# Kernel tuning notes

Measured on AMD Instinct MI355X. Metric: run time of the kernel, lower is better.

The kernel has to match this reference:

```python
import jax, jax.numpy as jnp
import numpy as np

N_NODES = 100000
N_EDGES = 1600000
IN_DIM = 256
HIDDEN = 128
N_CLASSES = 10


def setup_inputs() -> dict:
    key = jax.random.key(0)
    k1, k2, k3, k4 = jax.random.split(key, 4)
    x = jax.random.normal(k1, (N_NODES, IN_DIM), dtype=jnp.float32)
    edge_index = jax.random.randint(k2, (2, N_EDGES), 0, N_NODES, dtype=jnp.int64)
    # Glorot-ish init for weights
    W1 = jax.random.normal(k3, (IN_DIM, HIDDEN), dtype=jnp.float32) * (1.0 / np.sqrt(IN_DIM))
    b1 = jnp.zeros((HIDDEN,), dtype=jnp.float32)
    W2 = jax.random.normal(k4, (HIDDEN, N_CLASSES), dtype=jnp.float32) * (1.0 / np.sqrt(HIDDEN))
    b2 = jnp.zeros((N_CLASSES,), dtype=jnp.float32)
    return {"x": x, "edge_index": edge_index, "W1": W1, "b1": b1, "W2": W2, "b2": b2}


def _gcn_norm(edge_index, num_nodes):
    # PyG gcn_norm with add_self_loops=False, edge_weight=1:
    # deg over destination (col), norm = d^-1/2[src] * d^-1/2[dst]
    row, col = edge_index[0], edge_index[1]
    deg = jax.ops.segment_sum(jnp.ones((edge_index.shape[1],), jnp.float32), col,
                              num_segments=num_nodes)
    dinv = jnp.where(deg > 0, jax.lax.rsqrt(jnp.maximum(deg, 1.0)), 0.0)
    return dinv[row] * dinv[col]


def _gcn_conv(x, W, b, row, col, norm, num_nodes):
    h = x @ W                              # [N, out] dense transform
    msg = h[row] * norm[:, None]           # gather + scale, [E, out]
    out = jax.ops.segment_sum(msg, col, num_segments=num_nodes)  # scatter-add
    return out + b


def reference(x, edge_index, W1, b1, W2, b2):
    row, col = edge_index[0], edge_index[1]
    norm = _gcn_norm(edge_index, N_NODES)
    h = _gcn_conv(x, W1, b1, row, col, norm, N_NODES)
    h = jax.nn.relu(h)  # dropout is identity in eval mode
    out = _gcn_conv(h, W2, b2, row, col, norm, N_NODES)
    return out
```

## Files before the change

### kernel.cpp

```cpp
#include <hip/hip_runtime.h>
#include <hip/hip_fp16.h>

typedef _Float16 f16x8 __attribute__((ext_vector_type(8)));
typedef _Float16 f16x2 __attribute__((ext_vector_type(2)));
typedef float f32x4 __attribute__((ext_vector_type(4)));

#define NBUK_MAX 512
#define CHUNK 4096
#define BUKCAP 6144
#define WPAD 264
#define W1T_BLOCKS 64
#define BSTR 16


__global__ __launch_bounds__(512) void k_fat1(const float* __restrict__ W1,
                                              __half* __restrict__ W1T,
                                              const int* __restrict__ row,
                                              const int* __restrict__ col,
                                              int* __restrict__ bcur,
                                              unsigned* __restrict__ pairs,
                                              int E, int nbuk) {
    __shared__ int hist[NBUK_MAX];
    __shared__ int scanA[NBUK_MAX];
    __shared__ int scanB[NBUK_MAX];
    __shared__ int cur[NBUK_MAX];
    __shared__ int gpos[NBUK_MAX];
    __shared__ unsigned staged[CHUNK];
    int tid = threadIdx.x;

    if (blockIdx.x < W1T_BLOCKS) {
        int idx = blockIdx.x * 512 + tid;
        int c = idx >> 8, k = idx & 255;
        W1T[(size_t)c * 256 + k] = __float2half(W1[(size_t)k * 128 + c]);
        return;
    }

    int bid = blockIdx.x - W1T_BLOCKS;
    int e0 = bid * CHUNK;
    int nv = E - e0; if (nv > CHUNK) nv = CHUNK;

    hist[tid] = 0;
    __syncthreads();
    if (nv == CHUNK) {
        const int4* c4 = (const int4*)(col + e0);
#pragma unroll
        for (int it = 0; it < 2; ++it) {
            int4 v = c4[tid + it * 512];
            atomicAdd(&hist[v.x >> 8], 1);
            atomicAdd(&hist[v.y >> 8], 1);
            atomicAdd(&hist[v.z >> 8], 1);
            atomicAdd(&hist[v.w >> 8], 1);
        }
    } else {
        for (int i = tid; i < nv; i += 512) atomicAdd(&hist[col[e0 + i] >> 8], 1);
    }
    __syncthreads();
    int hv = hist[tid];
    scanA[tid] = hv;
    __syncthreads();
    int* pa = scanA;
    int* pb = scanB;
    for (int off = 1; off < 512; off <<= 1) {
        pb[tid] = pa[tid] + ((tid >= off) ? pa[tid - off] : 0);
        __syncthreads();
        int* sw = pa; pa = pb; pb = sw;
    }
    int ex = pa[tid] - hv;
    __syncthreads();
    pb[tid] = ex;
    cur[tid] = ex;
    if (tid < nbuk && hv > 0) gpos[tid] = atomicAdd(&bcur[tid * BSTR], hv);
    __syncthreads();
    int* excl = pb;
    if (nv == CHUNK) {
        const int4* c4 = (const int4*)(col + e0);
        const int4* r4 = (const int4*)(row + e0);
#pragma unroll
        for (int it = 0; it < 2; ++it) {
            int4 c = c4[tid + it * 512];
            int4 r = r4[tid + it * 512];
            int rk;
            rk = atomicAdd(&cur[c.x >> 8], 1); staged[rk] = ((unsigned)(c.x & 255) << 17) | (unsigned)r.x;
            rk = atomicAdd(&cur[c.y >> 8], 1); staged[rk] = ((unsigned)(c.y & 255) << 17) | (unsigned)r.y;
            rk = atomicAdd(&cur[c.z >> 8], 1); staged[rk] = ((unsigned)(c.z & 255) << 17) | (unsigned)r.z;
            rk = atomicAdd(&cur[c.w >> 8], 1); staged[rk] = ((unsigned)(c.w & 255) << 17) | (unsigned)r.w;
        }
    } else {
        for (int i = tid; i < nv; i += 512) {
            int c = col[e0 + i], r = row[e0 + i];
            int rk = atomicAdd(&cur[c >> 8], 1);
            staged[rk] = ((unsigned)(c & 255) << 17) | (unsigned)r;
        }
    }
    __syncthreads();
    int grp = tid >> 4, l16 = tid & 15;
    for (int b = grp; b < nbuk; b += 32) {
        int cnt = hist[b];
        if (cnt == 0) continue;
        int bs = excl[b];
        int gp = gpos[b];
        unsigned* dst = pairs + (size_t)b * BUKCAP;
        for (int l = l16; l < cnt; l += 16) {
            int d = gp + l;
            if (d < BUKCAP) dst[d] = staged[bs + l];
        }
    }
}


__global__ __launch_bounds__(256) void k_csr2a(const unsigned* __restrict__ pairs,
                                               const int* __restrict__ bcur,
                                               int* __restrict__ colptr,
                                               float* __restrict__ dinv,
                                               int N, int E) {
    __shared__ int fc[256];
    __shared__ int cp[256];
    __shared__ int tp[256];
    __shared__ int sA[NBUK_MAX];
    __shared__ int sB[NBUK_MAX];
    int b = blockIdx.x;
    int c0 = b << 8;
    int tid = threadIdx.x;
    fc[tid] = 0;
#pragma unroll
    for (int q = 0; q < 2; ++q) {
        int i = tid + q * 256;
        sA[i] = bcur[i * BSTR];
    }
    __syncthreads();
    int* pa = sA;
    int* pb = sB;
    for (int off = 1; off < 512; off <<= 1) {
#pragma unroll
        for (int q = 0; q < 2; ++q) {
            int i = tid + q * 256;
            pb[i] = pa[i] + ((i >= off) ? pa[i - off] : 0);
        }
        __syncthreads();
        int* sw = pa; pa = pb; pb = sw;
    }
    int cntb = bcur[b * BSTR];
    int p0 = pa[b] - cntb;
    int cnt = cntb > BUKCAP ? BUKCAP : cntb;
    __syncthreads();

    const unsigned* pbk = pairs + (size_t)b * BUKCAP;
    for (int i = tid; i < cnt; i += 256) {
        atomicAdd(&fc[pbk[i] >> 17], 1);
    }
    __syncthreads();
    int deg = fc[tid];
    cp[tid] = deg;
    __syncthreads();
    pa = cp; pb = tp;
    for (int off = 1; off < 256; off <<= 1) {
        pb[tid] = pa[tid] + ((tid >= off) ? pa[tid - off] : 0);
        __syncthreads();
        int* sw = pa; pa = pb; pb = sw;
    }
    int excl = pa[tid] - deg;
    if (c0 + tid < N) {
        colptr[c0 + tid] = p0 + excl;
        dinv[c0 + tid] = (deg > 0) ? rsqrtf((float)deg) : 0.0f;
    }
    if (b == 0 && tid == 0) colptr[N] = E;
}


#define SMEM_BYTES (128 * WPAD * 2)

__global__ __launch_bounds__(512, 4) void k_fat2(const unsigned* __restrict__ pairs,
                                                 const int* __restrict__ bcur,
                                                 const int* __restrict__ colptr,
                                                 int* __restrict__ srcs,
                                                 const float* __restrict__ x,
                                                 const __half* __restrict__ W1T,
                                                 const float* __restrict__ dinv,
                                                 __half* __restrict__ h,
                                                 int N, int nbuk) {
    __shared__ __align__(16) char smem[SMEM_BYTES];
    int tid = threadIdx.x;

    if (blockIdx.x < nbuk) {
        int* tp  = (int*)smem;
        int* fc  = tp + 256;
        int* loc = fc + 256;
        int b = blockIdx.x;
        int c0 = b << 8;
        int cnt = bcur[b * BSTR];
        if (cnt > BUKCAP) cnt = BUKCAP;
        int p0 = colptr[c0];
        if (tid < 256) {
            fc[tid] = 0;
            tp[tid] = (c0 + tid < N) ? (colptr[c0 + tid] - p0) : 0;
        }
        __syncthreads();
        const unsigned* pbk = pairs + (size_t)b * BUKCAP;
        for (int i = tid; i < cnt; i += 512) {
            unsigned v = pbk[i];
            int cl = (int)(v >> 17);
            int r = (int)(v & 0x1FFFFu);
            int off = tp[cl] + atomicAdd(&fc[cl], 1);
            if (off < BUKCAP) loc[off] = r;
            else srcs[p0 + off] = r;
        }
        __syncthreads();
        for (int i = tid; i < cnt; i += 512) srcs[p0 + i] = loc[i];
        return;
    }

    __half (*wt)[WPAD] = (__half(*)[WPAD])smem;
    int gb = blockIdx.x - nbuk;
    int w = tid >> 6, l = tid & 63;
    int r16 = l & 15, kg = l >> 4;
    int r0 = gb * 128;
    int rowi = r0 + w * 16 + r16;
    int rl = (rowi < N) ? rowi : 0;
    const float4* xp = (const float4*)x + (size_t)rl * 64 + kg * 2;

    float4 xr[8];
#pragma unroll
    for (int p = 0; p < 4; ++p) {
        xr[2 * p]     = xp[p * 8];
        xr[2 * p + 1] = xp[p * 8 + 1];
    }

#pragma unroll
    for (int it = 0; it < 8; ++it) {
        int idx = tid + it * 512;
        int c = idx >> 5, q = idx & 31;
        *(float4*)&wt[c][q * 8] = ((const float4*)W1T)[(size_t)c * 32 + q];
    }
    __syncthreads();

    f32x4 acc[8];
#pragma unroll
    for (int n = 0; n < 8; ++n) acc[n] = (f32x4){0.f, 0.f, 0.f, 0.f};

#pragma unroll
    for (int ks = 0; ks < 8; ++ks) {
        float4 c0 = xr[2 * (ks & 3)];
        float4 c1 = xr[2 * (ks & 3) + 1];
        if (ks < 4) {
            xr[2 * (ks & 3)]     = xp[(ks + 4) * 8];
            xr[2 * (ks & 3) + 1] = xp[(ks + 4) * 8 + 1];
        }
        f16x8 a;
        a[0] = (_Float16)c0.x; a[1] = (_Float16)c0.y;
        a[2] = (_Float16)c0.z; a[3] = (_Float16)c0.w;
        a[4] = (_Float16)c1.x; a[5] = (_Float16)c1.y;
        a[6] = (_Float16)c1.z; a[7] = (_Float16)c1.w;
        int kk = ks * 32;
#pragma unroll
        for (int n = 0; n < 8; ++n) {
            f16x8 b = *(const f16x8*)&wt[n * 16 + r16][kk + kg * 8];
            acc[n] = __builtin_amdgcn_mfma_f32_16x16x32_f16(a, b, acc[n], 0, 0, 0);
        }
    }

    float dn[4];
#pragma unroll
    for (int rr = 0; rr < 4; ++rr) {
        int r = r0 + w * 16 + kg * 4 + rr;
        dn[rr] = (r < N) ? dinv[r] : 0.f;
    }
#pragma unroll
    for (int n = 0; n < 8; ++n)
#pragma unroll
        for (int rr = 0; rr < 4; ++rr) {
            int r = r0 + w * 16 + kg * 4 + rr;
            if (r < N)
                h[(size_t)r * 128 + n * 16 + r16] = __float2half(dn[rr] * acc[n][rr]);
        }
}


#define LOAD8(sv, k, vv) { \
    int s0_ = __shfl(sv, (k) + 0), s1_ = __shfl(sv, (k) + 1); \
    int s2_ = __shfl(sv, (k) + 2), s3_ = __shfl(sv, (k) + 3); \
    int s4_ = __shfl(sv, (k) + 4), s5_ = __shfl(sv, (k) + 5); \
    int s6_ = __shfl(sv, (k) + 6), s7_ = __shfl(sv, (k) + 7); \
    vv[0] = hp[(size_t)s0_ * 64 + lane]; vv[1] = hp[(size_t)s1_ * 64 + lane]; \
    vv[2] = hp[(size_t)s2_ * 64 + lane]; vv[3] = hp[(size_t)s3_ * 64 + lane]; \
    vv[4] = hp[(size_t)s4_ * 64 + lane]; vv[5] = hp[(size_t)s5_ * 64 + lane]; \
    vv[6] = hp[(size_t)s6_ * 64 + lane]; vv[7] = hp[(size_t)s7_ * 64 + lane]; }

#define ACC8(vv, A0, A1) { \
    float2 f0_ = __half22float2(vv[0]), f1_ = __half22float2(vv[1]); \
    float2 f2_ = __half22float2(vv[2]), f3_ = __half22float2(vv[3]); \
    float2 f4_ = __half22float2(vv[4]), f5_ = __half22float2(vv[5]); \
    float2 f6_ = __half22float2(vv[6]), f7_ = __half22float2(vv[7]); \
    A0 += ((f0_.x + f1_.x) + (f2_.x + f3_.x)) + ((f4_.x + f5_.x) + (f6_.x + f7_.x)); \
    A1 += ((f0_.y + f1_.y) + (f2_.y + f3_.y)) + ((f4_.y + f5_.y) + (f6_.y + f7_.y)); }

__global__ __launch_bounds__(256) void k_agg1(const __half* __restrict__ h,
                                              const float* __restrict__ dinv,
                                              const int* __restrict__ colptr,
                                              const int* __restrict__ srcs,
                                              const float* __restrict__ b1,
                                              const float* __restrict__ W2,
                                              __half* __restrict__ t, int N) {
    __shared__ __half hs[64][136];
    __shared__ __half w2t[10][136];
    int tid = threadIdx.x;
    int wave = tid >> 6;
    int lane = tid & 63;

    for (int i = tid; i < 1280; i += 256) {
        int c = i >> 7, k = i & 127;
        w2t[c][k] = __float2half(W2[(size_t)k * 10 + c]);
    }

    const __half2* hp = (const __half2*)h;
    int nb0 = blockIdx.x * 64;
    float bb0 = b1[2 * lane], bb1 = b1[2 * lane + 1];

#pragma unroll 1
    for (int i = 0; i < 16; ++i) {
        int n = nb0 + wave * 16 + i;
        if (n >= N) break;
        int jb = colptr[n], je = colptr[n + 1];
        int len = je - jb;
        float a0 = 0.f, a1 = 0.f;
        for (int j0 = 0; j0 < len; j0 += 64) {
            int cnt = len - j0;
            if (cnt > 64) cnt = 64;
            int sv = (lane < cnt) ? srcs[jb + j0 + lane] : 0;
            int k = 0;
            for (; k + 8 <= cnt; k += 8) {
                __half2 va[8];
                LOAD8(sv, k, va);
                ACC8(va, a0, a1);
            }
            for (; k < cnt; ++k) {
                int s = __shfl(sv, k);
                float2 f = __half22float2(hp[(size_t)s * 64 + lane]);
                a0 += f.x; a1 += f.y;
            }
        }
        float dn = dinv[n];
        float v0 = dn * a0 + bb0;
        float v1 = dn * a1 + bb1;
        v0 = v0 > 0.f ? v0 : 0.f;
        v1 = v1 > 0.f ? v1 : 0.f;
        ((__half2*)&hs[wave * 16 + i][0])[lane] = __floats2half2_rn(v0, v1);
    }
    __syncthreads();

#pragma unroll
    for (int it = 0; it < 4; ++it) {
        int idx = tid + it * 256;
        int r = idx >> 4, c = idx & 15;
        int n = nb0 + r;
        if (n < N) {
            float s = 0.f;
            if (c < 10) {
                const float4* hr4 = (const float4*)&hs[r][0];
                const float4* wr4 = (const float4*)&w2t[c][0];
#pragma unroll
                for (int j = 0; j < 16; ++j) {
                    union { float4 v; f16x2 h2[4]; } uh, uw;
                    uh.v = hr4[j];
                    uw.v = wr4[j];
                    s = __builtin_amdgcn_fdot2(uh.h2[0], uw.h2[0], s, false);
                    s = __builtin_amdgcn_fdot2(uh.h2[1], uw.h2[1], s, false);
                    s = __builtin_amdgcn_fdot2(uh.h2[2], uw.h2[2], s, false);
                    s = __builtin_amdgcn_fdot2(uh.h2[3], uw.h2[3], s, false);
                }
                s *= dinv[n];
            }
            t[(size_t)n * 16 + c] = __float2half(s);
        }
    }
}


__global__ __launch_bounds__(256) void k_agg2(const __half* __restrict__ t,
                                              const float* __restrict__ dinv,
                                              const int* __restrict__ colptr,
                                              const int* __restrict__ srcs,
                                              const float* __restrict__ b2,
                                              float* __restrict__ out, int N) {
    int g = threadIdx.x >> 4;
    int lane16 = threadIdx.x & 15;
    int wg = g & 3;
    int n = blockIdx.x * 16 + g;
    if (n >= N) return;
    int jb = colptr[n], je = colptr[n + 1];
    float a = 0.f;
    for (int j0 = jb; j0 < je; j0 += 16) {
        int cnt = je - j0;
        if (cnt > 16) cnt = 16;
        int sv = (lane16 < cnt) ? srcs[j0 + lane16] : 0;
        int k = 0;
        for (; k + 8 <= cnt; k += 8) {
            int s0 = __shfl(sv, wg * 16 + k + 0);
            int s1 = __shfl(sv, wg * 16 + k + 1);
            int s2 = __shfl(sv, wg * 16 + k + 2);
            int s3 = __shfl(sv, wg * 16 + k + 3);
            int s4 = __shfl(sv, wg * 16 + k + 4);
            int s5 = __shfl(sv, wg * 16 + k + 5);
            int s6 = __shfl(sv, wg * 16 + k + 6);
            int s7 = __shfl(sv, wg * 16 + k + 7);
            float x0 = __half2float(t[(size_t)s0 * 16 + lane16]);
            float x1 = __half2float(t[(size_t)s1 * 16 + lane16]);
            float x2 = __half2float(t[(size_t)s2 * 16 + lane16]);
            float x3 = __half2float(t[(size_t)s3 * 16 + lane16]);
            float x4 = __half2float(t[(size_t)s4 * 16 + lane16]);
            float x5 = __half2float(t[(size_t)s5 * 16 + lane16]);
            float x6 = __half2float(t[(size_t)s6 * 16 + lane16]);
            float x7 = __half2float(t[(size_t)s7 * 16 + lane16]);
            a += ((x0 + x1) + (x2 + x3)) + ((x4 + x5) + (x6 + x7));
        }
        for (; k < cnt; ++k) {
            int s = __shfl(sv, wg * 16 + k);
            a += __half2float(t[(size_t)s * 16 + lane16]);
        }
    }
    if (lane16 < 10) out[(size_t)n * 10 + lane16] = dinv[n] * a + b2[lane16];
}


static inline size_t alignup(size_t x) { return (x + 255) & ~(size_t)255; }

extern "C" void kernel_launch(void* const* d_in, const int* in_sizes, int n_in,
                              void* d_out, int out_size, void* d_ws, size_t ws_size,
                              hipStream_t stream) {
    const float* x  = (const float*)d_in[0];
    const int*   ei = (const int*)d_in[1];
    const float* W1 = (const float*)d_in[2];
    const float* b1 = (const float*)d_in[3];
    const float* W2 = (const float*)d_in[4];
    const float* b2 = (const float*)d_in[5];

    int E = in_sizes[1] / 2;
    int N = in_sizes[0] / 256;
    const int* row = ei;
    const int* col = ei + E;
    int nbuk = (N + 255) >> 8;
    int nbE = (E + CHUNK - 1) / CHUNK;
    int nbG1 = (N + 127) / 128;

    char* ws = (char*)d_ws;
    size_t off = 0;
    int*      colptr = (int*)(ws + off);      off += alignup((size_t)(N + 1) * 4);
    float*    dinv   = (float*)(ws + off);    off += alignup((size_t)N * 4);
    int*      bcur   = (int*)(ws + off);      off += alignup((size_t)NBUK_MAX * BSTR * 4);
    int*      srcs   = (int*)(ws + off);      off += alignup((size_t)E * 4);
    unsigned* pairs  = (unsigned*)(ws + off); off += alignup((size_t)NBUK_MAX * BUKCAP * 4);
    __half*   W1T    = (__half*)(ws + off);   off += alignup((size_t)128 * 256 * 2);
    __half*   h      = (__half*)(ws + off);   off += alignup((size_t)N * 128 * 2);
    __half*   t      = (__half*)(ws + off);   off += alignup((size_t)N * 16 * 2);

    hipMemsetAsync(bcur, 0, (size_t)NBUK_MAX * BSTR * 4, stream);

    k_fat1<<<W1T_BLOCKS + nbE, 512, 0, stream>>>(W1, W1T, row, col, bcur, pairs, E, nbuk);
    k_csr2a<<<nbuk, 256, 0, stream>>>(pairs, bcur, colptr, dinv, N, E);
    k_fat2<<<nbuk + nbG1, 512, 0, stream>>>(pairs, bcur, colptr, srcs,
                                            x, W1T, dinv, h, N, nbuk);
    k_agg1<<<(N + 63) / 64, 256, 0, stream>>>(h, dinv, colptr, srcs, b1, W2, t, N);
    k_agg2<<<(N + 15) / 16, 256, 0, stream>>>(t, dinv, colptr, srcs, b2, (float*)d_out, N);
}
```

Baseline: 163.3 us.

## Fuse CSR colptr/dinv build into fat2 and apply source norm during aggregation

Removes the separate k_csr2a launch by having the bucket blocks of k_fat2 compute the bucket prefix scan, per-column degrees, colptr and dinv themselves before scattering sources. Because dinv is no longer ready when the GEMM blocks run, the per-row source normalization moves out of the GEMM epilogue into k_agg1, which gathers dinv[src] per edge and applies it as a weight. This saves one kernel launch and its sync point, at the cost of an extra per-edge dinv gather and multiply in the aggregation, plus redundant 512-entry scans in every bucket block. It also drops the overflow fallback write to srcs for offsets beyond BUKCAP.

Result: faster. 152.2 us (-6.8%).

```diff
diff --git a/kernel.cpp b/kernel.cpp
--- a/kernel.cpp
+++ b/kernel.cpp
@@ -108,101 +108,78 @@
 }
 
 
-__global__ __launch_bounds__(256) void k_csr2a(const unsigned* __restrict__ pairs,
-                                               const int* __restrict__ bcur,
-                                               int* __restrict__ colptr,
-                                               float* __restrict__ dinv,
-                                               int N, int E) {
-    __shared__ int fc[256];
-    __shared__ int cp[256];
-    __shared__ int tp[256];
-    __shared__ int sA[NBUK_MAX];
-    __shared__ int sB[NBUK_MAX];
-    int b = blockIdx.x;
-    int c0 = b << 8;
-    int tid = threadIdx.x;
-    fc[tid] = 0;
-#pragma unroll
-    for (int q = 0; q < 2; ++q) {
-        int i = tid + q * 256;
-        sA[i] = bcur[i * BSTR];
-    }
-    __syncthreads();
-    int* pa = sA;
-    int* pb = sB;
-    for (int off = 1; off < 512; off <<= 1) {
-#pragma unroll
-        for (int q = 0; q < 2; ++q) {
-            int i = tid + q * 256;
-            pb[i] = pa[i] + ((i >= off) ? pa[i - off] : 0);
-        }
-        __syncthreads();
-        int* sw = pa; pa = pb; pb = sw;
-    }
-    int cntb = bcur[b * BSTR];
-    int p0 = pa[b] - cntb;
-    int cnt = cntb > BUKCAP ? BUKCAP : cntb;
-    __syncthreads();
-
-    const unsigned* pbk = pairs + (size_t)b * BUKCAP;
-    for (int i = tid; i < cnt; i += 256) {
-        atomicAdd(&fc[pbk[i] >> 17], 1);
-    }
-    __syncthreads();
-    int deg = fc[tid];
-    cp[tid] = deg;
-    __syncthreads();
-    pa = cp; pb = tp;
-    for (int off = 1; off < 256; off <<= 1) {
-        pb[tid] = pa[tid] + ((tid >= off) ? pa[tid - off] : 0);
-        __syncthreads();
-        int* sw = pa; pa = pb; pb = sw;
-    }
-    int excl = pa[tid] - deg;
-    if (c0 + tid < N) {
-        colptr[c0 + tid] = p0 + excl;
-        dinv[c0 + tid] = (deg > 0) ? rsqrtf((float)deg) : 0.0f;
-    }
-    if (b == 0 && tid == 0) colptr[N] = E;
-}
-
-
 #define SMEM_BYTES (128 * WPAD * 2)
 
 __global__ __launch_bounds__(512, 4) void k_fat2(const unsigned* __restrict__ pairs,
                                                  const int* __restrict__ bcur,
-                                                 const int* __restrict__ colptr,
+                                                 int* __restrict__ colptr,
+                                                 float* __restrict__ dinv,
                                                  int* __restrict__ srcs,
                                                  const float* __restrict__ x,
                                                  const __half* __restrict__ W1T,
-                                                 const float* __restrict__ dinv,
                                                  __half* __restrict__ h,
-                                                 int N, int nbuk) {
+                                                 int N, int E, int nbuk) {
     __shared__ __align__(16) char smem[SMEM_BYTES];
     int tid = threadIdx.x;
 
     if (blockIdx.x < nbuk) {
-        int* tp  = (int*)smem;
-        int* fc  = tp + 256;
-        int* loc = fc + 256;
+        int* sA  = (int*)smem;
+        int* sB  = sA + 512;
+        int* fc  = sB + 512;
+        int* tpE = fc + 256;
+        int* loc = tpE + 256;
         int b = blockIdx.x;
         int c0 = b << 8;
-        int cnt = bcur[b * BSTR];
-        if (cnt > BUKCAP) cnt = BUKCAP;
-        int p0 = colptr[c0];
+
+        sA[tid] = bcur[tid * BSTR];
+        if (tid < 256) fc[tid] = 0;
+        __syncthreads();
+        int* pa = sA;
+        int* pb = sB;
+        for (int off = 1; off < 512; off <<= 1) {
+            pb[tid] = pa[tid] + ((tid >= off) ? pa[tid - off] : 0);
+            __syncthreads();
+            int* sw = pa; pa = pb; pb = sw;
+        }
+        int cntb = bcur[b * BSTR];
+        int p0 = pa[b] - cntb;
+        int cnt = cntb > BUKCAP ? BUKCAP : cntb;
+        __syncthreads();
+
+        const unsigned* pbk = pairs + (size_t)b * BUKCAP;
+        for (int i = tid; i < cnt; i += 512) {
+            atomicAdd(&fc[pbk[i] >> 17], 1);
+        }
+        __syncthreads();
+        int deg = (tid < 256) ? fc[tid] : 0;
+        if (tid < 256) sA[tid] = deg;
+        __syncthreads();
+        pa = sA; pb = sB;
+        for (int off = 1; off < 256; off <<= 1) {
+            int v = 0;
+            if (tid < 256) v = pa[tid] + ((tid >= off) ? pa[tid - off] : 0);
+            __syncthreads();
+            if (tid < 256) pb[tid] = v;
+            __syncthreads();
+            int* sw = pa; pa = pb; pb = sw;
+        }
         if (tid < 256) {
+            int excl = pa[tid] - deg;
+            tpE[tid] = excl;
             fc[tid] = 0;
-            tp[tid] = (c0 + tid < N) ? (colptr[c0 + tid] - p0) : 0;
-        }
-        __syncthreads();
-        const unsigned* pbk = pairs + (size_t)b * BUKCAP;
+            if (c0 + tid < N) {
+                colptr[c0 + tid] = p0 + excl;
+                dinv[c0 + tid] = (deg > 0) ? rsqrtf((float)deg) : 0.0f;
+            }
+        }
+        if (b == 0 && tid == 0) colptr[N] = E;
+        __syncthreads();
         for (int i = tid; i < cnt; i += 512) {
             unsigned v = pbk[i];
             int cl = (int)(v >> 17);
             int r = (int)(v & 0x1FFFFu);
-            int off = tp[cl] + atomicAdd(&fc[cl], 1);
+            int off = tpE[cl] + atomicAdd(&fc[cl], 1);
             if (off < BUKCAP) loc[off] = r;
-            else srcs[p0 + off] = r;
         }
         __syncthreads();
         for (int i = tid; i < cnt; i += 512) srcs[p0 + i] = loc[i];
@@ -258,40 +235,40 @@
         }
     }
 
-    float dn[4];
-#pragma unroll
-    for (int rr = 0; rr < 4; ++rr) {
-        int r = r0 + w * 16 + kg * 4 + rr;
-        dn[rr] = (r < N) ? dinv[r] : 0.f;
-    }
 #pragma unroll
     for (int n = 0; n < 8; ++n)
 #pragma unroll
         for (int rr = 0; rr < 4; ++rr) {
             int r = r0 + w * 16 + kg * 4 + rr;
             if (r < N)
-                h[(size_t)r * 128 + n * 16 + r16] = __float2half(dn[rr] * acc[n][rr]);
+                h[(size_t)r * 128 + n * 16 + r16] = __float2half(acc[n][rr]);
         }
 }
 
 
-#define LOAD8(sv, k, vv) { \
+#define LOAD8W(sv, dv, k, vv, ww) { \
     int s0_ = __shfl(sv, (k) + 0), s1_ = __shfl(sv, (k) + 1); \
     int s2_ = __shfl(sv, (k) + 2), s3_ = __shfl(sv, (k) + 3); \
     int s4_ = __shfl(sv, (k) + 4), s5_ = __shfl(sv, (k) + 5); \
     int s6_ = __shfl(sv, (k) + 6), s7_ = __shfl(sv, (k) + 7); \
+    ww[0] = __shfl(dv, (k) + 0); ww[1] = __shfl(dv, (k) + 1); \
+    ww[2] = __shfl(dv, (k) + 2); ww[3] = __shfl(dv, (k) + 3); \
+    ww[4] = __shfl(dv, (k) + 4); ww[5] = __shfl(dv, (k) + 5); \
+    ww[6] = __shfl(dv, (k) + 6); ww[7] = __shfl(dv, (k) + 7); \
     vv[0] = hp[(size_t)s0_ * 64 + lane]; vv[1] = hp[(size_t)s1_ * 64 + lane]; \
     vv[2] = hp[(size_t)s2_ * 64 + lane]; vv[3] = hp[(size_t)s3_ * 64 + lane]; \
     vv[4] = hp[(size_t)s4_ * 64 + lane]; vv[5] = hp[(size_t)s5_ * 64 + lane]; \
     vv[6] = hp[(size_t)s6_ * 64 + lane]; vv[7] = hp[(size_t)s7_ * 64 + lane]; }
 
-#define ACC8(vv, A0, A1) { \
+#define ACC8W(vv, ww, A0, A1) { \
     float2 f0_ = __half22float2(vv[0]), f1_ = __half22float2(vv[1]); \
     float2 f2_ = __half22float2(vv[2]), f3_ = __half22float2(vv[3]); \
     float2 f4_ = __half22float2(vv[4]), f5_ = __half22float2(vv[5]); \
     float2 f6_ = __half22float2(vv[6]), f7_ = __half22float2(vv[7]); \
-    A0 += ((f0_.x + f1_.x) + (f2_.x + f3_.x)) + ((f4_.x + f5_.x) + (f6_.x + f7_.x)); \
-    A1 += ((f0_.y + f1_.y) + (f2_.y + f3_.y)) + ((f4_.y + f5_.y) + (f6_.y + f7_.y)); }
+    A0 += ((ww[0]*f0_.x + ww[1]*f1_.x) + (ww[2]*f2_.x + ww[3]*f3_.x)) \
+        + ((ww[4]*f4_.x + ww[5]*f5_.x) + (ww[6]*f6_.x + ww[7]*f7_.x)); \
+    A1 += ((ww[0]*f0_.y + ww[1]*f1_.y) + (ww[2]*f2_.y + ww[3]*f3_.y)) \
+        + ((ww[4]*f4_.y + ww[5]*f5_.y) + (ww[6]*f6_.y + ww[7]*f7_.y)); }
 
 __global__ __launch_bounds__(256) void k_agg1(const __half* __restrict__ h,
                                               const float* __restrict__ dinv,
@@ -326,16 +303,19 @@
             int cnt = len - j0;
             if (cnt > 64) cnt = 64;
             int sv = (lane < cnt) ? srcs[jb + j0 + lane] : 0;
+            float dv = (lane < cnt) ? dinv[sv] : 0.f;
             int k = 0;
             for (; k + 8 <= cnt; k += 8) {
                 __half2 va[8];
-                LOAD8(sv, k, va);
-                ACC8(va, a0, a1);
+                float wa[8];
+                LOAD8W(sv, dv, k, va, wa);
+                ACC8W(va, wa, a0, a1);
             }
             for (; k < cnt; ++k) {
                 int s = __shfl(sv, k);
+                float wgt = __shfl(dv, k);
                 float2 f = __half22float2(hp[(size_t)s * 64 + lane]);
-                a0 += f.x; a1 += f.y;
+                a0 += wgt * f.x; a1 += wgt * f.y;
             }
         }
         float dn = dinv[n];
@@ -455,9 +435,8 @@
     hipMemsetAsync(bcur, 0, (size_t)NBUK_MAX * BSTR * 4, stream);
 
     k_fat1<<<W1T_BLOCKS + nbE, 512, 0, stream>>>(W1, W1T, row, col, bcur, pairs, E, nbuk);
-    k_csr2a<<<nbuk, 256, 0, stream>>>(pairs, bcur, colptr, dinv, N, E);
-    k_fat2<<<nbuk + nbG1, 512, 0, stream>>>(pairs, bcur, colptr, srcs,
-                                            x, W1T, dinv, h, N, nbuk);
+    k_fat2<<<nbuk + nbG1, 512, 0, stream>>>(pairs, bcur, colptr, dinv, srcs,
+                                            x, W1T, h, N, E, nbuk);
     k_agg1<<<(N + 63) / 64, 256, 0, stream>>>(h, dinv, colptr, srcs, b1, W2, t, N);
     k_agg2<<<(N + 15) / 16, 256, 0, stream>>>(t, dinv, colptr, srcs, b2, (float*)d_out, N);
 }
```
